# Kernel tuning notes

Hardware: AMD Instinct MI355X
Metric: run time of the kernel (lower is better)

Reference implementation:

```python
import jax, jax.numpy as jnp
import numpy as np

OBS_LEN = 8
PRED_LEN = 12
BATCH = 65536
EMB = 64
H = 64


def setup_inputs() -> dict:
    key = jax.random.key(0)
    ks = jax.random.split(key, 18)
    s = 1.0 / np.sqrt(H)  # torch default uniform bound scale, used as std here

    def p(k, shape):
        return (jax.random.normal(k, shape, dtype=jnp.float32) * s).astype(jnp.float32)

    return {
        "obs_traj": jax.random.normal(ks[0], (OBS_LEN, BATCH, 2), dtype=jnp.float32),
        "obs_traj_rel": jax.random.normal(ks[1], (OBS_LEN, BATCH, 2), dtype=jnp.float32),
        # encoder params
        "enc_emb_w": p(ks[2], (EMB, 2)),
        "enc_emb_b": p(ks[3], (EMB,)),
        "enc_w_ih": p(ks[4], (4 * H, EMB)),
        "enc_w_hh": p(ks[5], (4 * H, H)),
        "enc_b_ih": p(ks[6], (4 * H,)),
        "enc_b_hh": p(ks[7], (4 * H,)),
        # decoder params
        "dec_emb_w": p(ks[8], (EMB, 2)),
        "dec_emb_b": p(ks[9], (EMB,)),
        "dec_w_ih": p(ks[10], (4 * H, EMB)),
        "dec_w_hh": p(ks[11], (4 * H, H)),
        "dec_b_ih": p(ks[12], (4 * H,)),
        "dec_b_hh": p(ks[13], (4 * H,)),
        "h2p_w": p(ks[14], (2, H)),
        "h2p_b": p(ks[15], (2,)),
    }


def _lstm_cell(h, c, x, w_ih, w_hh, b_ih, b_hh):
    # torch nn.LSTM gate order: i, f, g, o
    gates = x @ w_ih.T + h @ w_hh.T + (b_ih + b_hh)
    i, f, g, o = jnp.split(gates, 4, axis=-1)
    c_new = jax.nn.sigmoid(f) * c + jax.nn.sigmoid(i) * jnp.tanh(g)
    h_new = jax.nn.sigmoid(o) * jnp.tanh(c_new)
    return h_new, c_new


def reference(obs_traj, obs_traj_rel,
              enc_emb_w, enc_emb_b, enc_w_ih, enc_w_hh, enc_b_ih, enc_b_hh,
              dec_emb_w, dec_emb_b, dec_w_ih, dec_w_hh, dec_b_ih, dec_b_hh,
              h2p_w, h2p_b):
    batch = obs_traj_rel.shape[1]

    # ---------- Encoder ----------
    enc_in = obs_traj_rel @ enc_emb_w.T + enc_emb_b  # [T, B, EMB]

    def enc_step(carry, x_t):
        h, c = carry
        h, c = _lstm_cell(h, c, x_t, enc_w_ih, enc_w_hh, enc_b_ih, enc_b_hh)
        return (h, c), None

    h0 = jnp.zeros((batch, H), dtype=obs_traj_rel.dtype)
    c0 = jnp.zeros((batch, H), dtype=obs_traj_rel.dtype)
    (h_enc, _), _ = jax.lax.scan(enc_step, (h0, c0), enc_in)

    # ---------- Decoder ----------
    dec_h = h_enc                                   # final encoder hidden seeds decoder
    dec_c = jnp.zeros((batch, H), dtype=obs_traj_rel.dtype)
    last_pos_rel = obs_traj_rel[-1]
    dec_in = last_pos_rel @ dec_emb_w.T + dec_emb_b  # [B, EMB]

    def dec_step(carry, _):
        h, c, x = carry
        h, c = _lstm_cell(h, c, x, dec_w_ih, dec_w_hh, dec_b_ih, dec_b_hh)
        rel_pos = h @ h2p_w.T + h2p_b               # [B, 2]
        x_next = rel_pos @ dec_emb_w.T + dec_emb_b  # [B, EMB]
        return (h, c, x_next), rel_pos

    (_, _, _), pred_traj_fake_rel = jax.lax.scan(
        dec_step, (dec_h, dec_c, dec_in), None, length=PRED_LEN)
    return pred_traj_fake_rel  # [PRED_LEN, B, 2]
```

## Files before the change

kernel.cpp:

```cpp
#include <hip/hip_runtime.h>

#define OBS_LEN 8
#define PRED_LEN 12
#define NTHREADS 256

typedef __attribute__((ext_vector_type(8))) short short8;
typedef __attribute__((ext_vector_type(4))) float floatx4;
typedef __attribute__((ext_vector_type(2))) float floatx2;
typedef __attribute__((ext_vector_type(4))) unsigned int u32x4;
typedef __attribute__((ext_vector_type(2))) unsigned int u32x2;
typedef unsigned short u16;
typedef unsigned int u32;

#define L2E 1.442695040888963f

__device__ __forceinline__ u16 f2bf(float f) {
  __bf16 b = (__bf16)f;
  return __builtin_bit_cast(u16, b);
}
__device__ __forceinline__ float bf2f(u16 h) {
  return __builtin_bit_cast(float, ((u32)h) << 16);
}
__device__ __forceinline__ float rndbf(float f) { return (float)(__bf16)f; }

#if __has_builtin(__builtin_amdgcn_exp2f)
__device__ __forceinline__ float fexp2_(float x) { return __builtin_amdgcn_exp2f(x); }
#else
__device__ __forceinline__ float fexp2_(float x) { return exp2f(x); }
#endif
__device__ __forceinline__ floatx2 exp2v(floatx2 x) {
  floatx2 r;
  r.x = fexp2_(x.x);
  r.y = fexp2_(x.y);
  return r;
}
#if __has_builtin(__builtin_amdgcn_rcpf)
__device__ __forceinline__ floatx2 rcp2(floatx2 x) {
  floatx2 r;
  r.x = __builtin_amdgcn_rcpf(x.x);
  r.y = __builtin_amdgcn_rcpf(x.y);
  return r;
}
#else
__device__ __forceinline__ floatx2 rcp2(floatx2 x) {
  return floatx2{1.0f / x.x, 1.0f / x.y};
}
#endif

__device__ __forceinline__ floatx4 mfma_bf(short8 a, short8 b, floatx4 c) {
  return __builtin_amdgcn_mfma_f32_16x16x32_bf16(a, b, c, 0, 0, 0);
}

__device__ __forceinline__ void stage_w(const float* __restrict__ W,
                                        u16* __restrict__ dst, int tid) {
  const float* src = W + tid * 64;
  u16* d = dst + tid * 64;
  const int rs = tid & 7;
#pragma unroll
  for (int b = 0; b < 8; ++b) {
    const floatx4 w0 = *(const floatx4*)(src + b * 8);
    const floatx4 w1 = *(const floatx4*)(src + b * 8 + 4);
    short8 v;
#pragma unroll
    for (int j = 0; j < 4; ++j) {
      v[j] = (short)f2bf(w0[j]);
      v[j + 4] = (short)f2bf(w1[j]);
    }
    *(short8*)(d + ((b ^ rs) * 8)) = v;
  }
}

template <bool REL>
__device__ __forceinline__ void step(
    u16* __restrict__ hw,
    const u16* __restrict__ whhS, const u16* __restrict__ wihS,
    const float* __restrict__ biasS,
    const u32* __restrict__ ewpkS, const float* __restrict__ ebvS,
    const float* __restrict__ posrow,
    const short8 (&aex)[2], floatx2 (&c)[4][2],
    float* __restrict__ outp, float b2p0, float b2p1,
    int q, int l16) {
  const int sw = l16 & 7;
  const u16* hr = hw + l16 * 64;
  const short8 hb0 = *(const short8*)(hr + ((q ^ sw) * 8));
  const short8 hb1 = *(const short8*)(hr + (((4 + q) ^ sw) * 8));
  float rb0, rb1;
  if (REL) {
    floatx4 z = {0.f, 0.f, 0.f, 0.f};
    z = mfma_bf(aex[0], hb0, z);
    z = mfma_bf(aex[1], hb1, z);
    const float r0 = __shfl(z[0], l16) + b2p0;
    const float r1 = __shfl(z[1], l16) + b2p1;
    if (q == 0) *(floatx2*)(outp + l16 * 2) = floatx2{r0, r1};
    rb0 = rndbf(r0);
    rb1 = rndbf(r1);
  } else {
    const floatx2 rr = *(const floatx2*)(posrow + l16 * 2);
    rb0 = rndbf(rr.x);
    rb1 = rndbf(rr.y);
  }
  short8 xb0, xb1;
  {
    const u32x4 e0a = *(const u32x4*)(ewpkS + q * 8);
    const u32x4 e0b = *(const u32x4*)(ewpkS + q * 8 + 4);
    const u32x4 e1a = *(const u32x4*)(ewpkS + 32 + q * 8);
    const u32x4 e1b = *(const u32x4*)(ewpkS + 32 + q * 8 + 4);
    const floatx4 b0a = *(const floatx4*)(ebvS + q * 8);
    const floatx4 b0b = *(const floatx4*)(ebvS + q * 8 + 4);
    const floatx4 b1a = *(const floatx4*)(ebvS + 32 + q * 8);
    const floatx4 b1b = *(const floatx4*)(ebvS + 32 + q * 8 + 4);
#pragma unroll
    for (int j = 0; j < 4; ++j) {
      u32 p = e0a[j];
      xb0[j] = (short)f2bf(rb0 * bf2f((u16)(p & 0xffffu)) +
                           (rb1 * bf2f((u16)(p >> 16)) + b0a[j]));
      p = e0b[j];
      xb0[j + 4] = (short)f2bf(rb0 * bf2f((u16)(p & 0xffffu)) +
                               (rb1 * bf2f((u16)(p >> 16)) + b0b[j]));
      p = e1a[j];
      xb1[j] = (short)f2bf(rb0 * bf2f((u16)(p & 0xffffu)) +
                           (rb1 * bf2f((u16)(p >> 16)) + b1a[j]));
      p = e1b[j];
      xb1[j + 4] = (short)f2bf(rb0 * bf2f((u16)(p & 0xffffu)) +
                               (rb1 * bf2f((u16)(p >> 16)) + b1b[j]));
    }
  }
#pragma unroll 1
  for (int tq = 0; tq < 4; ++tq) {
    const int rbase = tq * 16 + l16;
    floatx4 acc[4];
#pragma unroll
    for (int gt = 0; gt < 4; ++gt) {
      const floatx4 bias = *(const floatx4*)(biasS + gt * 64 + tq * 16 + q * 4);
      const short8 ah0 =
          *(const short8*)(whhS + (gt * 64 + rbase) * 64 + ((q ^ sw) * 8));
      acc[gt] = mfma_bf(ah0, hb0, bias);
    }
#pragma unroll
    for (int gt = 0; gt < 4; ++gt) {
      const short8 ax0 =
          *(const short8*)(wihS + (gt * 64 + rbase) * 64 + ((q ^ sw) * 8));
      acc[gt] = mfma_bf(ax0, xb0, acc[gt]);
    }
#pragma unroll
    for (int gt = 0; gt < 4; ++gt) {
      const short8 ah1 =
          *(const short8*)(whhS + (gt * 64 + rbase) * 64 + (((4 + q) ^ sw) * 8));
      acc[gt] = mfma_bf(ah1, hb1, acc[gt]);
    }
#pragma unroll
    for (int gt = 0; gt < 4; ++gt) {
      const short8 ax1 =
          *(const short8*)(wihS + (gt * 64 + rbase) * 64 + (((4 + q) ^ sw) * 8));
      acc[gt] = mfma_bf(ax1, xb1, acc[gt]);
    }
    u32 hpk[2];
#pragma unroll
    for (int p = 0; p < 2; ++p) {
      const floatx2 iv = {acc[0][2 * p], acc[0][2 * p + 1]};
      const floatx2 fv = {acc[1][2 * p], acc[1][2 * p + 1]};
      const floatx2 gv = {acc[2][2 * p], acc[2][2 * p + 1]};
      const floatx2 ov = {acc[3][2 * p], acc[3][2 * p + 1]};
      const floatx2 ei = exp2v(iv * -L2E);
      const floatx2 ef = exp2v(fv * -L2E);
      const floatx2 eg = exp2v(gv * (2.0f * L2E));
      const floatx2 eo = exp2v(ov * -L2E);
      const floatx2 A = ei + 1.0f;
      const floatx2 F = ef + 1.0f;
      const floatx2 Bg = eg + 1.0f;
      const floatx2 P = A * Bg;
      const floatx2 num = c[tq][p] * P + (eg - 1.0f) * F;
      const floatx2 cn = num * rcp2(F * P);
      c[tq][p] = cn;
      const floatx2 ec = exp2v(cn * (2.0f * L2E));
      const floatx2 h = (ec - 1.0f) * rcp2((eo + 1.0f) * (ec + 1.0f));
      hpk[p] = (u32)f2bf(h.x) | ((u32)f2bf(h.y) << 16);
    }
    *(u32x2*)(hw + l16 * 64 + (((2 * tq + (q >> 1)) ^ sw) * 8) + (q & 1) * 4) =
        u32x2{hpk[0], hpk[1]};
  }
}

__global__ void __launch_bounds__(NTHREADS, 2)
lstm_kernel(const float* __restrict__ obs_rel,
            const float* __restrict__ enc_emb_w, const float* __restrict__ enc_emb_b,
            const float* __restrict__ enc_w_ih, const float* __restrict__ enc_w_hh,
            const float* __restrict__ enc_b_ih, const float* __restrict__ enc_b_hh,
            const float* __restrict__ dec_emb_w, const float* __restrict__ dec_emb_b,
            const float* __restrict__ dec_w_ih, const float* __restrict__ dec_w_hh,
            const float* __restrict__ dec_b_ih, const float* __restrict__ dec_b_hh,
            const float* __restrict__ h2p_w, const float* __restrict__ h2p_b,
            float* __restrict__ out, int batch) {
  __shared__ __align__(16) u16 whhS[256 * 64];
  __shared__ __align__(16) u16 wihS[256 * 64];
  __shared__ __align__(16) u16 hS[4][16 * 64];
  __shared__ __align__(16) float biasS[256];
  __shared__ __align__(16) u32 ewpkS[64];
  __shared__ __align__(16) float ebvS[64];

  const int tid = threadIdx.x;
  const int wv = tid >> 6, lane = tid & 63;
  const int q = lane >> 4, l16 = lane & 15;
  const long S0 = (long)blockIdx.x * 64;

  stage_w(enc_w_hh, whhS, tid);
  stage_w(enc_w_ih, wihS, tid);
  biasS[tid] = enc_b_ih[tid] + enc_b_hh[tid];
  if (tid < 64) {
    ewpkS[tid] = (u32)f2bf(enc_emb_w[tid * 2]) |
                 ((u32)f2bf(enc_emb_w[tid * 2 + 1]) << 16);
    ebvS[tid] = enc_emb_b[tid];
  }
  for (int i = tid; i < 4 * 16 * 64 / 2; i += NTHREADS) ((u32*)&hS[0][0])[i] = 0;

  short8 aex[2];
  floatx2 c[4][2];
#pragma unroll
  for (int t = 0; t < 4; ++t) c[t][0] = c[t][1] = floatx2{0.f, 0.f};
  aex[0] = aex[1] = short8{0, 0, 0, 0, 0, 0, 0, 0};
  const float b2p0 = h2p_b[0], b2p1 = h2p_b[1];
  u16* hw = &hS[wv][0];
  __syncthreads();

#pragma unroll 1
  for (int t = 0; t < OBS_LEN; ++t)
    step<false>(hw, whhS, wihS, biasS, ewpkS, ebvS,
                obs_rel + (long)t * batch * 2 + (S0 + wv * 16) * 2,
                aex, c, nullptr, b2p0, b2p1, q, l16);

  __syncthreads();
  stage_w(dec_w_hh, whhS, tid);
  stage_w(dec_w_ih, wihS, tid);
  biasS[tid] = dec_b_ih[tid] + dec_b_hh[tid];
  if (tid < 64) {
    ewpkS[tid] = (u32)f2bf(dec_emb_w[tid * 2]) |
                 ((u32)f2bf(dec_emb_w[tid * 2 + 1]) << 16);
    ebvS[tid] = dec_emb_b[tid];
  }
  __syncthreads();
#pragma unroll
  for (int t = 0; t < 4; ++t) c[t][0] = c[t][1] = floatx2{0.f, 0.f};
#pragma unroll
  for (int kf = 0; kf < 2; ++kf) {
    short8 a = {0, 0, 0, 0, 0, 0, 0, 0};
    if (l16 < 2) {
      const float* src = h2p_w + l16 * 64 + kf * 32 + q * 8;
#pragma unroll
      for (int j = 0; j < 8; ++j) a[j] = (short)f2bf(src[j]);
    }
    aex[kf] = a;
  }

  step<false>(hw, whhS, wihS, biasS, ewpkS, ebvS,
              obs_rel + (long)7 * batch * 2 + (S0 + wv * 16) * 2,
              aex, c, nullptr, b2p0, b2p1, q, l16);

#pragma unroll 1
  for (int j = 1; j < PRED_LEN; ++j)
    step<true>(hw, whhS, wihS, biasS, ewpkS, ebvS, nullptr, aex, c,
               out + (long)(j - 1) * batch * 2 + (S0 + wv * 16) * 2,
               b2p0, b2p1, q, l16);

  {
    const int sw = l16 & 7;
    const u16* hr = hw + l16 * 64;
    const short8 hb0 = *(const short8*)(hr + ((q ^ sw) * 8));
    const short8 hb1 = *(const short8*)(hr + (((4 + q) ^ sw) * 8));
    floatx4 z = {0.f, 0.f, 0.f, 0.f};
    z = mfma_bf(aex[0], hb0, z);
    z = mfma_bf(aex[1], hb1, z);
    if (q == 0) {
      float* outp = out + (long)(PRED_LEN - 1) * batch * 2 + (S0 + wv * 16) * 2;
      *(floatx2*)(outp + l16 * 2) = floatx2{z[0] + b2p0, z[1] + b2p1};
    }
  }
}

extern "C" void kernel_launch(void* const* d_in, const int* in_sizes, int n_in,
                              void* d_out, int out_size, void* d_ws, size_t ws_size,
                              hipStream_t stream) {
  const float* obs_rel = (const float*)d_in[1];
  const int batch = in_sizes[1] / (OBS_LEN * 2);

  const int blocks = batch / 64;
  hipLaunchKernelGGL(lstm_kernel, dim3(blocks), dim3(NTHREADS), 0, stream,
                     obs_rel,
                     (const float*)d_in[2], (const float*)d_in[3],
                     (const float*)d_in[4], (const float*)d_in[5],
                     (const float*)d_in[6], (const float*)d_in[7],
                     (const float*)d_in[8], (const float*)d_in[9],
                     (const float*)d_in[10], (const float*)d_in[11],
                     (const float*)d_in[12], (const float*)d_in[13],
                     (const float*)d_in[14], (const float*)d_in[15],
                     (float*)d_out, batch);
}
```

Before: 240.3 us.

## Process two batch tiles per wave and precompute biases in a prep kernel

Each block now handles 128 sequences instead of 64, with each wave interleaving two 16-row tiles (A and B) that have separate hidden-state buffers and cell states. The bf16 weight staging into LDS is therefore amortized over twice as many sequences, and the block count is halved. Bias sums and packed embedding weights move to a tiny prep kernel writing to workspace, and step reads them from global memory instead of LDS. This raises register pressure from the doubled cell state and adds an extra kernel launch.

```diff
diff --git a/kernel.cpp b/kernel.cpp
--- a/kernel.cpp
+++ b/kernel.cpp
@@ -74,8 +74,8 @@
 __device__ __forceinline__ void step(
     u16* __restrict__ hw,
     const u16* __restrict__ whhS, const u16* __restrict__ wihS,
-    const float* __restrict__ biasS,
-    const u32* __restrict__ ewpkS, const float* __restrict__ ebvS,
+    const float* __restrict__ biasG,
+    const u32* __restrict__ ewpkG, const float* __restrict__ ebvG,
     const float* __restrict__ posrow,
     const short8 (&aex)[2], floatx2 (&c)[4][2],
     float* __restrict__ outp, float b2p0, float b2p1,
@@ -101,14 +101,14 @@
   }
   short8 xb0, xb1;
   {
-    const u32x4 e0a = *(const u32x4*)(ewpkS + q * 8);
-    const u32x4 e0b = *(const u32x4*)(ewpkS + q * 8 + 4);
-    const u32x4 e1a = *(const u32x4*)(ewpkS + 32 + q * 8);
-    const u32x4 e1b = *(const u32x4*)(ewpkS + 32 + q * 8 + 4);
-    const floatx4 b0a = *(const floatx4*)(ebvS + q * 8);
-    const floatx4 b0b = *(const floatx4*)(ebvS + q * 8 + 4);
-    const floatx4 b1a = *(const floatx4*)(ebvS + 32 + q * 8);
-    const floatx4 b1b = *(const floatx4*)(ebvS + 32 + q * 8 + 4);
+    const u32x4 e0a = *(const u32x4*)(ewpkG + q * 8);
+    const u32x4 e0b = *(const u32x4*)(ewpkG + q * 8 + 4);
+    const u32x4 e1a = *(const u32x4*)(ewpkG + 32 + q * 8);
+    const u32x4 e1b = *(const u32x4*)(ewpkG + 32 + q * 8 + 4);
+    const floatx4 b0a = *(const floatx4*)(ebvG + q * 8);
+    const floatx4 b0b = *(const floatx4*)(ebvG + q * 8 + 4);
+    const floatx4 b1a = *(const floatx4*)(ebvG + 32 + q * 8);
+    const floatx4 b1b = *(const floatx4*)(ebvG + 32 + q * 8 + 4);
 #pragma unroll
     for (int j = 0; j < 4; ++j) {
       u32 p = e0a[j];
@@ -131,7 +131,7 @@
     floatx4 acc[4];
 #pragma unroll
     for (int gt = 0; gt < 4; ++gt) {
-      const floatx4 bias = *(const floatx4*)(biasS + gt * 64 + tq * 16 + q * 4);
+      const floatx4 bias = *(const floatx4*)(biasG + gt * 64 + tq * 16 + q * 4);
       const short8 ah0 =
           *(const short8*)(whhS + (gt * 64 + rbase) * 64 + ((q ^ sw) * 8));
       acc[gt] = mfma_bf(ah0, hb0, bias);
@@ -181,65 +181,84 @@
   }
 }
 
+__global__ void prep_kernel(const float* __restrict__ eew, const float* __restrict__ eeb,
+                            const float* __restrict__ ebi, const float* __restrict__ ebh,
+                            const float* __restrict__ dew, const float* __restrict__ deb,
+                            const float* __restrict__ dbi, const float* __restrict__ dbh,
+                            float* __restrict__ ws) {
+  const int t = threadIdx.x;
+  ws[t] = ebi[t] + ebh[t];
+  ws[256 + t] = dbi[t] + dbh[t];
+  if (t < 64) {
+    ((u32*)ws)[512 + t] =
+        (u32)f2bf(eew[t * 2]) | ((u32)f2bf(eew[t * 2 + 1]) << 16);
+    ((u32*)ws)[576 + t] =
+        (u32)f2bf(dew[t * 2]) | ((u32)f2bf(dew[t * 2 + 1]) << 16);
+    ws[640 + t] = eeb[t];
+    ws[704 + t] = deb[t];
+  }
+}
+
 __global__ void __launch_bounds__(NTHREADS, 2)
 lstm_kernel(const float* __restrict__ obs_rel,
-            const float* __restrict__ enc_emb_w, const float* __restrict__ enc_emb_b,
             const float* __restrict__ enc_w_ih, const float* __restrict__ enc_w_hh,
-            const float* __restrict__ enc_b_ih, const float* __restrict__ enc_b_hh,
-            const float* __restrict__ dec_emb_w, const float* __restrict__ dec_emb_b,
             const float* __restrict__ dec_w_ih, const float* __restrict__ dec_w_hh,
-            const float* __restrict__ dec_b_ih, const float* __restrict__ dec_b_hh,
             const float* __restrict__ h2p_w, const float* __restrict__ h2p_b,
+            const float* __restrict__ ws,
             float* __restrict__ out, int batch) {
   __shared__ __align__(16) u16 whhS[256 * 64];
   __shared__ __align__(16) u16 wihS[256 * 64];
-  __shared__ __align__(16) u16 hS[4][16 * 64];
-  __shared__ __align__(16) float biasS[256];
-  __shared__ __align__(16) u32 ewpkS[64];
-  __shared__ __align__(16) float ebvS[64];
+  __shared__ __align__(16) u16 hS[4][2][16 * 64];
 
   const int tid = threadIdx.x;
   const int wv = tid >> 6, lane = tid & 63;
   const int q = lane >> 4, l16 = lane & 15;
-  const long S0 = (long)blockIdx.x * 64;
+  const long S0 = (long)blockIdx.x * 128;
+  const long sA = S0 + wv * 32, sB = sA + 16;
 
   stage_w(enc_w_hh, whhS, tid);
   stage_w(enc_w_ih, wihS, tid);
-  biasS[tid] = enc_b_ih[tid] + enc_b_hh[tid];
-  if (tid < 64) {
-    ewpkS[tid] = (u32)f2bf(enc_emb_w[tid * 2]) |
-                 ((u32)f2bf(enc_emb_w[tid * 2 + 1]) << 16);
-    ebvS[tid] = enc_emb_b[tid];
-  }
-  for (int i = tid; i < 4 * 16 * 64 / 2; i += NTHREADS) ((u32*)&hS[0][0])[i] = 0;
+  for (int i = tid; i < 4 * 2 * 16 * 64 / 2; i += NTHREADS)
+    ((u32*)&hS[0][0][0])[i] = 0;
+
+  const float* biasE = ws;
+  const float* biasD = ws + 256;
+  const u32* ewpkE = (const u32*)ws + 512;
+  const u32* ewpkD = (const u32*)ws + 576;
+  const float* ebvE = ws + 640;
+  const float* ebvD = ws + 704;
 
   short8 aex[2];
-  floatx2 c[4][2];
-#pragma unroll
-  for (int t = 0; t < 4; ++t) c[t][0] = c[t][1] = floatx2{0.f, 0.f};
+  floatx2 cA[4][2], cB[4][2];
+#pragma unroll
+  for (int t = 0; t < 4; ++t) {
+    cA[t][0] = cA[t][1] = floatx2{0.f, 0.f};
+    cB[t][0] = cB[t][1] = floatx2{0.f, 0.f};
+  }
   aex[0] = aex[1] = short8{0, 0, 0, 0, 0, 0, 0, 0};
   const float b2p0 = h2p_b[0], b2p1 = h2p_b[1];
-  u16* hw = &hS[wv][0];
+  u16* hwA = &hS[wv][0][0];
+  u16* hwB = &hS[wv][1][0];
   __syncthreads();
 
 #pragma unroll 1
-  for (int t = 0; t < OBS_LEN; ++t)
-    step<false>(hw, whhS, wihS, biasS, ewpkS, ebvS,
-                obs_rel + (long)t * batch * 2 + (S0 + wv * 16) * 2,
-                aex, c, nullptr, b2p0, b2p1, q, l16);
+  for (int t = 0; t < OBS_LEN; ++t) {
+    const float* prow = obs_rel + (long)t * batch * 2;
+    step<false>(hwA, whhS, wihS, biasE, ewpkE, ebvE, prow + sA * 2,
+                aex, cA, nullptr, b2p0, b2p1, q, l16);
+    step<false>(hwB, whhS, wihS, biasE, ewpkE, ebvE, prow + sB * 2,
+                aex, cB, nullptr, b2p0, b2p1, q, l16);
+  }
 
   __syncthreads();
   stage_w(dec_w_hh, whhS, tid);
   stage_w(dec_w_ih, wihS, tid);
-  biasS[tid] = dec_b_ih[tid] + dec_b_hh[tid];
-  if (tid < 64) {
-    ewpkS[tid] = (u32)f2bf(dec_emb_w[tid * 2]) |
-                 ((u32)f2bf(dec_emb_w[tid * 2 + 1]) << 16);
-    ebvS[tid] = dec_emb_b[tid];
-  }
   __syncthreads();
 #pragma unroll
-  for (int t = 0; t < 4; ++t) c[t][0] = c[t][1] = floatx2{0.f, 0.f};
+  for (int t = 0; t < 4; ++t) {
+    cA[t][0] = cA[t][1] = floatx2{0.f, 0.f};
+    cB[t][0] = cB[t][1] = floatx2{0.f, 0.f};
+  }
 #pragma unroll
   for (int kf = 0; kf < 2; ++kf) {
     short8 a = {0, 0, 0, 0, 0, 0, 0, 0};
@@ -251,27 +270,38 @@
     aex[kf] = a;
   }
 
-  step<false>(hw, whhS, wihS, biasS, ewpkS, ebvS,
-              obs_rel + (long)7 * batch * 2 + (S0 + wv * 16) * 2,
-              aex, c, nullptr, b2p0, b2p1, q, l16);
+  {
+    const float* prow = obs_rel + (long)7 * batch * 2;
+    step<false>(hwA, whhS, wihS, biasD, ewpkD, ebvD, prow + sA * 2,
+                aex, cA, nullptr, b2p0, b2p1, q, l16);
+    step<false>(hwB, whhS, wihS, biasD, ewpkD, ebvD, prow + sB * 2,
+                aex, cB, nullptr, b2p0, b2p1, q, l16);
+  }
 
 #pragma unroll 1
-  for (int j = 1; j < PRED_LEN; ++j)
-    step<true>(hw, whhS, wihS, biasS, ewpkS, ebvS, nullptr, aex, c,
-               out + (long)(j - 1) * batch * 2 + (S0 + wv * 16) * 2,
-               b2p0, b2p1, q, l16);
+  for (int j = 1; j < PRED_LEN; ++j) {
+    float* orow = out + (long)(j - 1) * batch * 2;
+    step<true>(hwA, whhS, wihS, biasD, ewpkD, ebvD, nullptr, aex, cA,
+               orow + sA * 2, b2p0, b2p1, q, l16);
+    step<true>(hwB, whhS, wihS, biasD, ewpkD, ebvD, nullptr, aex, cB,
+               orow + sB * 2, b2p0, b2p1, q, l16);
+  }
 
   {
+    float* orow = out + (long)(PRED_LEN - 1) * batch * 2;
     const int sw = l16 & 7;
-    const u16* hr = hw + l16 * 64;
-    const short8 hb0 = *(const short8*)(hr + ((q ^ sw) * 8));
-    const short8 hb1 = *(const short8*)(hr + (((4 + q) ^ sw) * 8));
-    floatx4 z = {0.f, 0.f, 0.f, 0.f};
-    z = mfma_bf(aex[0], hb0, z);
-    z = mfma_bf(aex[1], hb1, z);
-    if (q == 0) {
-      float* outp = out + (long)(PRED_LEN - 1) * batch * 2 + (S0 + wv * 16) * 2;
-      *(floatx2*)(outp + l16 * 2) = floatx2{z[0] + b2p0, z[1] + b2p1};
+#pragma unroll
+    for (int g = 0; g < 2; ++g) {
+      const u16* hr = (g ? hwB : hwA) + l16 * 64;
+      const short8 hb0 = *(const short8*)(hr + ((q ^ sw) * 8));
+      const short8 hb1 = *(const short8*)(hr + (((4 + q) ^ sw) * 8));
+      floatx4 z = {0.f, 0.f, 0.f, 0.f};
+      z = mfma_bf(aex[0], hb0, z);
+      z = mfma_bf(aex[1], hb1, z);
+      if (q == 0) {
+        float* outp = orow + (g ? sB : sA) * 2;
+        *(floatx2*)(outp + l16 * 2) = floatx2{z[0] + b2p0, z[1] + b2p1};
+      }
     }
   }
 }
@@ -281,16 +311,19 @@
                               hipStream_t stream) {
   const float* obs_rel = (const float*)d_in[1];
   const int batch = in_sizes[1] / (OBS_LEN * 2);
-
-  const int blocks = batch / 64;
+  float* ws = (float*)d_ws;
+
+  hipLaunchKernelGGL(prep_kernel, dim3(1), dim3(256), 0, stream,
+                     (const float*)d_in[2], (const float*)d_in[3],
+                     (const float*)d_in[6], (const float*)d_in[7],
+                     (const float*)d_in[8], (const float*)d_in[9],
+                     (const float*)d_in[12], (const float*)d_in[13], ws);
+
+  const int blocks = batch / 128;
   hipLaunchKernelGGL(lstm_kernel, dim3(blocks), dim3(NTHREADS), 0, stream,
                      obs_rel,
-                     (const float*)d_in[2], (const float*)d_in[3],
                      (const float*)d_in[4], (const float*)d_in[5],
-                     (const float*)d_in[6], (const float*)d_in[7],
-                     (const float*)d_in[8], (const float*)d_in[9],
                      (const float*)d_in[10], (const float*)d_in[11],
-                     (const float*)d_in[12], (const float*)d_in[13],
                      (const float*)d_in[14], (const float*)d_in[15],
-                     (float*)d_out, batch);
-}
+                     ws, (float*)d_out, batch);
+}
```

New measurement: 235.7 us. Within noise of the previous version (-1.9%).
